# Performance work log

Measured on AMD Instinct MI355X. Metric: run time of the kernel, lower is better.

Reference implementation:

```python
import jax, jax.numpy as jnp
import numpy as np
import math

B, S, D = 16, 2048, 128
MASK_SENTINEL = -100

def setup_inputs() -> dict:
    key = jax.random.key(0)
    k1, k2, k3, k4 = jax.random.split(key, 4)
    value = jax.random.normal(k1, (B, S, D), dtype=jnp.float32)
    key_t = jax.random.normal(k2, (B, S, D), dtype=jnp.float32)
    query = jax.random.normal(k3, (B, S, D), dtype=jnp.float32)
    # mask uses -100 as the "masked out" sentinel, anything else is kept.
    bits = jax.random.randint(k4, (B, S, S), 0, 2, dtype=jnp.int32)
    mask = jnp.where(bits == 0, jnp.int32(MASK_SENTINEL), jnp.int32(0))
    return {"value": value, "key": key_t, "query": query, "mask": mask}

def reference(value, key, query, mask):
    # scores: [B, Sq, Sk]
    scale = 1.0 / math.sqrt(query.shape[-1])
    scores = jnp.einsum("bqd,bkd->bqk", query, key) * scale
    min_val = jnp.finfo(scores.dtype).min
    masked = jnp.where(mask == MASK_SENTINEL, min_val, scores)
    attn = jax.nn.softmax(masked, axis=-1)
    return jnp.einsum("bqk,bkd->bqd", attn, value)
```

## Files before the change

### kernel.cpp

```cpp
#include <hip/hip_runtime.h>
#include <hip/hip_bf16.h>

#define BATCH 16
#define SEQ   2048
#define DIM   128
#define QBLK  64
#define KVBLK 64
#define NT    (SEQ / KVBLK)
#define PPAD  72
#define L2E   1.4426950408889634f
#define THR   8.0f
#define MSENT -100

typedef __attribute__((ext_vector_type(8))) short bf16x8;
typedef __attribute__((ext_vector_type(4))) float f32x4;
typedef __attribute__((ext_vector_type(4))) int   i32x4;
typedef __attribute__((ext_vector_type(4))) unsigned u32x4;

__device__ __forceinline__ unsigned short f2bf(float f) {
  union { float f; unsigned u; } v; v.f = f;
  return (unsigned short)((v.u + 0x7FFFu + ((v.u >> 16) & 1u)) >> 16);
}
__device__ __forceinline__ unsigned packbf(float a, float b) {
  return ((unsigned)f2bf(b) << 16) | (unsigned)f2bf(a);
}

__global__ __launch_bounds__(256) void cvt_k(const float* __restrict__ K,
                                             short* __restrict__ Kb) {
  const size_t i = ((size_t)blockIdx.x * 256 + threadIdx.x) * 8;
  f32x4 a = __builtin_nontemporal_load((const f32x4*)(K + i));
  f32x4 b = __builtin_nontemporal_load((const f32x4*)(K + i + 4));
  u32x4 o = { packbf(a[0], a[1]), packbf(a[2], a[3]),
              packbf(b[0], b[1]), packbf(b[2], b[3]) };
  *(u32x4*)(Kb + i) = o;
}

__global__ __launch_bounds__(256) void cvt_vt(const float* __restrict__ V,
                                              short* __restrict__ Vt) {
  __shared__ unsigned t32[64][65];
  const int tid = threadIdx.x;
  const int b  = blockIdx.x >> 5;
  const int s0 = (blockIdx.x & 31) * 64;
  #pragma unroll
  for (int it = 0; it < 8; ++it) {
    const int idx = tid + it * 256;
    const int r = idx >> 5, c4 = idx & 31;
    f32x4 x = __builtin_nontemporal_load(
        (const f32x4*)(V + ((size_t)b * SEQ + s0 + r) * DIM + c4 * 4));
    t32[r][c4 * 2]     = packbf(x[0], x[1]);
    t32[r][c4 * 2 + 1] = packbf(x[2], x[3]);
  }
  __syncthreads();
  const int d = tid >> 1, sh = tid & 1;
  unsigned short outv[32];
  #pragma unroll
  for (int j = 0; j < 32; ++j) {
    const unsigned u = t32[sh * 32 + j][d >> 1];
    outv[j] = (d & 1) ? (unsigned short)(u >> 16) : (unsigned short)(u & 0xffff);
  }
  short* op = Vt + ((size_t)b * DIM + d) * SEQ + s0 + sh * 32;
  #pragma unroll
  for (int q = 0; q < 4; ++q) {
    bf16x8 y;
    #pragma unroll
    for (int j = 0; j < 8; ++j) y[j] = (short)outv[q * 8 + j];
    *(bf16x8*)(op + q * 8) = y;
  }
}

__device__ __forceinline__ void gload16(const void* g, void* l) {
  __builtin_amdgcn_global_load_lds(
      (const __attribute__((address_space(1))) unsigned*)g,
      (__attribute__((address_space(3))) unsigned*)l, 16, 0, 0);
}

__device__ __forceinline__ void stage_kv(const char* __restrict__ Kb2,
                                         const char* __restrict__ Vtb2,
                                         int k0, int w, int l,
                                         void* kbuf, void* vbuf) {
  #pragma unroll
  for (int it = 0; it < 4; ++it) {
    const int ch = w * 4 + it;
    const int r  = ch * 4 + (l >> 4);
    const int sg = (l & 15) ^ (r & 15);
    gload16(Kb2 + (size_t)(k0 + r) * 256 + sg * 16, (char*)kbuf + ch * 1024);
  }
  #pragma unroll
  for (int it = 0; it < 4; ++it) {
    const int ch = w * 4 + it;
    const int d2 = ch * 4 + (l >> 4);
    const int Su = (l & 15) ^ (d2 & 15);
    const int d  = 2 * d2 + (Su >> 3);
    const int m  = Su & 7;
    gload16(Vtb2 + (size_t)d * (SEQ * 2) + k0 * 2 + m * 16,
            (char*)vbuf + ch * 1024);
  }
}

__global__ __launch_bounds__(256, 2) void attn_fwd(
    const short* __restrict__ Kbf, const short* __restrict__ Vt,
    const float* __restrict__ Qg, const int* __restrict__ Mg,
    float* __restrict__ Og) {
  __shared__ short lds_k[2][KVBLK * DIM];
  __shared__ short lds_v[2][DIM * KVBLK];
  __shared__ short lds_p[4][16 * PPAD];

  const int tid = threadIdx.x;
  const int w   = tid >> 6;
  const int l   = tid & 63;
  const int g   = l >> 4;
  const int lr  = l & 15;

  const int blk = blockIdx.x;
  const int swz = (blk & 7) * 64 + (blk >> 3);
  const int b   = swz >> 5;
  const int q0  = (swz & 31) * QBLK;

  const float scale = 0.08838834764831845f;

  const char* Kb2  = (const char*)(Kbf + (size_t)b * SEQ * DIM);
  const char* Vtb2 = (const char*)(Vt  + (size_t)b * DIM * SEQ);
  const int*  Mr   = Mg + (size_t)b * SEQ * SEQ + (size_t)(q0 + w * 16 + lr) * SEQ;

  stage_kv(Kb2, Vtb2, 0, w, l, lds_k[0], lds_v[0]);
  __builtin_amdgcn_sched_barrier(0);

  bf16x8 qa[4];
  {
    const float* qbase = Qg + ((size_t)b * SEQ + (size_t)(q0 + w * 16 + lr)) * DIM + g * 8;
    #pragma unroll
    for (int kk = 0; kk < 4; ++kk) {
      f32x4 x0 = *(const f32x4*)(qbase + kk * 32);
      f32x4 x1 = *(const f32x4*)(qbase + kk * 32 + 4);
      bf16x8 f;
      #pragma unroll
      for (int j = 0; j < 4; ++j) {
        f[j]     = (short)f2bf(x0[j] * scale);
        f[j + 4] = (short)f2bf(x1[j] * scale);
      }
      qa[kk] = f;
    }
  }
  __builtin_amdgcn_sched_barrier(0);

  i32x4 mreg[4];
  #pragma unroll
  for (int sub = 0; sub < 4; ++sub)
    mreg[sub] = __builtin_nontemporal_load((const i32x4*)(Mr + 16 * sub + 4 * g));

  f32x4 acc[8];
  #pragma unroll
  for (int t = 0; t < 8; ++t) acc[t] = (f32x4){0.f, 0.f, 0.f, 0.f};
  float mrow = -1e30f, lsum = 0.f;

  asm volatile("s_waitcnt vmcnt(4)" ::: "memory");
  __builtin_amdgcn_s_barrier();

  int cur = 0;
  for (int t = 0; t < NT; ++t) {
    const int k0 = t * KVBLK;
    if (t + 1 < NT)
      stage_kv(Kb2, Vtb2, k0 + KVBLK, w, l, lds_k[cur ^ 1], lds_v[cur ^ 1]);
    __builtin_amdgcn_sched_barrier(0);

    const char* kbuf = (const char*)lds_k[cur];
    const char* vbuf = (const char*)lds_v[cur];

    f32x4 s[4];
    #pragma unroll
    for (int sub = 0; sub < 4; ++sub) s[sub] = (f32x4){0.f, 0.f, 0.f, 0.f};
    #pragma unroll
    for (int kk = 0; kk < 4; ++kk) {
      #pragma unroll
      for (int sub = 0; sub < 4; ++sub) {
        const int krow = sub * 16 + lr;
        const int cb = (64 * kk + 16 * g) ^ (lr << 4);
        bf16x8 kb = *(const bf16x8*)(kbuf + krow * 256 + cb);
        s[sub] = __builtin_amdgcn_mfma_f32_16x16x32_bf16(kb, qa[kk], s[sub], 0, 0, 0);
      }
    }

    #pragma unroll
    for (int sub = 0; sub < 4; ++sub)
      #pragma unroll
      for (int i = 0; i < 4; ++i)
        if (mreg[sub][i] == MSENT) s[sub][i] = -1e30f;
    if (t + 1 < NT) {
      #pragma unroll
      for (int sub = 0; sub < 4; ++sub)
        mreg[sub] = __builtin_nontemporal_load(
            (const i32x4*)(Mr + k0 + KVBLK + 16 * sub + 4 * g));
    }

    float tm = -1e30f;
    #pragma unroll
    for (int sub = 0; sub < 4; ++sub)
      #pragma unroll
      for (int i = 0; i < 4; ++i) tm = fmaxf(tm, s[sub][i]);
    tm = fmaxf(tm, __shfl_xor(tm, 16));
    tm = fmaxf(tm, __shfl_xor(tm, 32));
    if (__any(tm > mrow + THR)) {
      const float mnew = fmaxf(mrow, tm);
      const float al = __builtin_amdgcn_exp2f((mrow - mnew) * L2E);
      mrow = mnew; lsum *= al;
      float av[4];
      #pragma unroll
      for (int i = 0; i < 4; ++i) av[i] = __shfl(al, 4 * g + i);
      #pragma unroll
      for (int t8 = 0; t8 < 8; ++t8)
        #pragma unroll
        for (int i = 0; i < 4; ++i) acc[t8][i] *= av[i];
    }

    {
      unsigned* prow = (unsigned*)&lds_p[w][lr * PPAD];
      #pragma unroll
      for (int sub = 0; sub < 4; ++sub) {
        const float p0 = __builtin_amdgcn_exp2f((s[sub][0] - mrow) * L2E);
        const float p1 = __builtin_amdgcn_exp2f((s[sub][1] - mrow) * L2E);
        const float p2 = __builtin_amdgcn_exp2f((s[sub][2] - mrow) * L2E);
        const float p3 = __builtin_amdgcn_exp2f((s[sub][3] - mrow) * L2E);
        lsum += (p0 + p1) + (p2 + p3);
        prow[8 * sub + 2 * g]     = packbf(p0, p1);
        prow[8 * sub + 2 * g + 1] = packbf(p2, p3);
      }
    }

    bf16x8 pa[2];
    #pragma unroll
    for (int kk = 0; kk < 2; ++kk)
      pa[kk] = *(const bf16x8*)&lds_p[w][lr * PPAD + kk * 32 + g * 8];
    #pragma unroll
    for (int t8 = 0; t8 < 8; ++t8) {
      const int d2 = 8 * t8 + (lr >> 1);
      #pragma unroll
      for (int kk = 0; kk < 2; ++kk) {
        const int S = ((lr & 1) * 8 + 4 * kk + g) ^ (d2 & 15);
        bf16x8 vb = *(const bf16x8*)(vbuf + d2 * 256 + S * 16);
        acc[t8] = __builtin_amdgcn_mfma_f32_16x16x32_bf16(pa[kk], vb, acc[t8], 0, 0, 0);
      }
    }

    if (t + 1 < NT) {
      asm volatile("s_waitcnt vmcnt(4)" ::: "memory");
      __builtin_amdgcn_s_barrier();
    }
    cur ^= 1;
  }

  lsum += __shfl_xor(lsum, 16);
  lsum += __shfl_xor(lsum, 32);
  const float rden = 1.f / lsum;
  float rdv[4];
  #pragma unroll
  for (int i = 0; i < 4; ++i) rdv[i] = __shfl(rden, 4 * g + i);
  float* ob = Og + ((size_t)b * SEQ + (size_t)(q0 + w * 16)) * DIM;
  #pragma unroll
  for (int t8 = 0; t8 < 8; ++t8)
    #pragma unroll
    for (int i = 0; i < 4; ++i)
      ob[(4 * g + i) * DIM + 16 * t8 + lr] = acc[t8][i] * rdv[i];
}

extern "C" void kernel_launch(void* const* d_in, const int* in_sizes, int n_in,
                              void* d_out, int out_size, void* d_ws, size_t ws_size,
                              hipStream_t stream) {
  (void)in_sizes; (void)n_in; (void)out_size; (void)ws_size;
  const float* Vg = (const float*)d_in[0];
  const float* Kg = (const float*)d_in[1];
  const float* Qg = (const float*)d_in[2];
  const int*   Mg = (const int*)d_in[3];
  float* Og = (float*)d_out;

  short* Kbf = (short*)d_ws;
  short* Vt  = Kbf + (size_t)BATCH * SEQ * DIM;
  cvt_k<<<dim3(BATCH * SEQ * DIM / (8 * 256)), 256, 0, stream>>>(Kg, Kbf);
  cvt_vt<<<dim3(BATCH * (SEQ / 64)), 256, 0, stream>>>(Vg, Vt);
  attn_fwd<<<dim3(BATCH * (SEQ / QBLK)), 256, 0, stream>>>(Kbf, Vt, Qg, Mg, Og);
}
```

Before: 117.3 us.

## Split KV range across two blocks with merge kernel and LDS-staged mask

```diff
diff --git a/kernel.cpp b/kernel.cpp
--- a/kernel.cpp
+++ b/kernel.cpp
@@ -5,9 +5,8 @@
 #define SEQ   2048
 #define DIM   128
 #define QBLK  64
-#define KVBLK 64
-#define NT    (SEQ / KVBLK)
-#define PPAD  72
+#define KVB   32
+#define NTK   32
 #define L2E   1.4426950408889634f
 #define THR   8.0f
 #define MSENT -100
@@ -74,10 +73,218 @@
       (__attribute__((address_space(3))) unsigned*)l, 16, 0, 0);
 }
 
-__device__ __forceinline__ void stage_kv(const char* __restrict__ Kb2,
-                                         const char* __restrict__ Vtb2,
-                                         int k0, int w, int l,
-                                         void* kbuf, void* vbuf) {
+__device__ __forceinline__ void stage3(const char* __restrict__ Kb2,
+                                       const char* __restrict__ Vtb2,
+                                       const char* __restrict__ Mb2,
+                                       int k0, int w, int l,
+                                       void* kbuf, void* vbuf, void* mbuf) {
+  #pragma unroll
+  for (int it = 0; it < 2; ++it) {
+    const int ch = w * 2 + it;
+    const int r  = ch * 4 + (l >> 4);
+    const int sp = (l & 15) ^ (r & 15);
+    gload16(Kb2 + (size_t)(k0 + r) * 256 + sp * 16, (char*)kbuf + ch * 1024);
+  }
+  #pragma unroll
+  for (int it = 0; it < 2; ++it) {
+    const int ch = w * 2 + it;
+    const int d  = ch * 16 + (l >> 2);
+    const int sp = (l & 3) ^ ((l >> 3) & 3);
+    gload16(Vtb2 + (size_t)d * (SEQ * 2) + (size_t)k0 * 2 + sp * 16,
+            (char*)vbuf + ch * 1024);
+  }
+  #pragma unroll
+  for (int it = 0; it < 2; ++it) {
+    const int ch = w * 2 + it;
+    const int r  = ch * 8 + (l >> 3);
+    const int sp = (l & 7) ^ (l >> 3);
+    gload16(Mb2 + (size_t)r * (SEQ * 4) + (size_t)k0 * 4 + sp * 16,
+            (char*)mbuf + ch * 1024);
+  }
+}
+
+__global__ __launch_bounds__(256, 3) void attn_split(
+    const short* __restrict__ Kbf, const short* __restrict__ Vt,
+    const float* __restrict__ Qg, const int* __restrict__ Mg,
+    float* __restrict__ O0, float* __restrict__ O1, float2* __restrict__ ML) {
+  __shared__ short lds_k[2][KVB * DIM];
+  __shared__ short lds_v[2][DIM * KVB];
+  __shared__ int   lds_m[2][QBLK * KVB];
+
+  const int tid = threadIdx.x;
+  const int w = tid >> 6, l = tid & 63, g = l >> 4, lr = l & 15;
+
+  const int blk = blockIdx.x;
+  const int swz = (blk & 7) * 128 + (blk >> 3);
+  const int b   = swz >> 6;
+  const int x   = swz & 63;
+  const int h   = x >> 5;
+  const int q0  = (x & 31) * QBLK;
+  const int kvbase = h * (SEQ / 2);
+
+  const char* Kb2  = (const char*)(Kbf + (size_t)b * SEQ * DIM);
+  const char* Vtb2 = (const char*)(Vt  + (size_t)b * DIM * SEQ);
+  const char* Mb2  = (const char*)(Mg + (size_t)b * SEQ * SEQ + (size_t)q0 * SEQ);
+
+  stage3(Kb2, Vtb2, Mb2, kvbase, w, l, lds_k[0], lds_v[0], lds_m[0]);
+  __builtin_amdgcn_sched_barrier(0);
+
+  const float scale = 0.08838834764831845f;
+  bf16x8 qa[4];
+  {
+    const float* qbase = Qg + ((size_t)b * SEQ + (size_t)(q0 + w * 16 + lr)) * DIM + g * 8;
+    #pragma unroll
+    for (int kk = 0; kk < 4; ++kk) {
+      f32x4 x0 = *(const f32x4*)(qbase + kk * 32);
+      f32x4 x1 = *(const f32x4*)(qbase + kk * 32 + 4);
+      bf16x8 f;
+      #pragma unroll
+      for (int j = 0; j < 4; ++j) {
+        f[j]     = (short)f2bf(x0[j] * scale);
+        f[j + 4] = (short)f2bf(x1[j] * scale);
+      }
+      qa[kk] = f;
+    }
+  }
+  __builtin_amdgcn_sched_barrier(0);
+
+  f32x4 acc[8];
+  #pragma unroll
+  for (int t = 0; t < 8; ++t) acc[t] = (f32x4){0.f, 0.f, 0.f, 0.f};
+  float mrow = -1e30f, lsum = 0.f;
+
+  const int laneA = ((g & 1) << 5) + lr;
+  const int laneB = ((g & 1) << 5) + 16 + lr;
+
+  __syncthreads();
+  int cur = 0;
+
+  for (int t = 0; t < NTK; ++t) {
+    const int k0 = kvbase + t * KVB;
+    if (t + 1 < NTK)
+      stage3(Kb2, Vtb2, Mb2, k0 + KVB, w, l,
+             lds_k[cur ^ 1], lds_v[cur ^ 1], lds_m[cur ^ 1]);
+    __builtin_amdgcn_sched_barrier(0);
+
+    const char* kbuf = (const char*)lds_k[cur];
+    const char* vbuf = (const char*)lds_v[cur];
+    const char* mbuf = (const char*)lds_m[cur];
+
+    f32x4 s[2];
+    s[0] = (f32x4){0.f, 0.f, 0.f, 0.f};
+    s[1] = (f32x4){0.f, 0.f, 0.f, 0.f};
+    #pragma unroll
+    for (int kk = 0; kk < 4; ++kk) {
+      const int S = (((4 * kk + g) ^ lr) << 4);
+      bf16x8 kb0 = *(const bf16x8*)(kbuf + lr * 256 + S);
+      bf16x8 kb1 = *(const bf16x8*)(kbuf + (16 + lr) * 256 + S);
+      s[0] = __builtin_amdgcn_mfma_f32_16x16x32_bf16(kb0, qa[kk], s[0], 0, 0, 0);
+      s[1] = __builtin_amdgcn_mfma_f32_16x16x32_bf16(kb1, qa[kk], s[1], 0, 0, 0);
+    }
+
+    #pragma unroll
+    for (int sub = 0; sub < 2; ++sub) {
+      const i32x4 mm = *(const i32x4*)(
+          mbuf + (w * 16 + lr) * 128 + (((4 * sub + g) ^ (lr & 7)) << 4));
+      #pragma unroll
+      for (int i = 0; i < 4; ++i)
+        if (mm[i] == MSENT) s[sub][i] = -1e30f;
+    }
+
+    float tm = s[0][0];
+    tm = fmaxf(tm, s[0][1]); tm = fmaxf(tm, s[0][2]); tm = fmaxf(tm, s[0][3]);
+    tm = fmaxf(tm, s[1][0]); tm = fmaxf(tm, s[1][1]);
+    tm = fmaxf(tm, s[1][2]); tm = fmaxf(tm, s[1][3]);
+    tm = fmaxf(tm, __shfl_xor(tm, 16));
+    tm = fmaxf(tm, __shfl_xor(tm, 32));
+    if (__any(tm > mrow + THR)) {
+      const float mnew = fmaxf(mrow, tm);
+      const float al = __builtin_amdgcn_exp2f((mrow - mnew) * L2E);
+      mrow = mnew; lsum *= al;
+      float av[4];
+      #pragma unroll
+      for (int i = 0; i < 4; ++i) av[i] = __shfl(al, 4 * g + i);
+      #pragma unroll
+      for (int t8 = 0; t8 < 8; ++t8)
+        #pragma unroll
+        for (int i = 0; i < 4; ++i) acc[t8][i] *= av[i];
+    }
+
+    unsigned pk[2][2];
+    #pragma unroll
+    for (int sub = 0; sub < 2; ++sub) {
+      const float p0 = __builtin_amdgcn_exp2f((s[sub][0] - mrow) * L2E);
+      const float p1 = __builtin_amdgcn_exp2f((s[sub][1] - mrow) * L2E);
+      const float p2 = __builtin_amdgcn_exp2f((s[sub][2] - mrow) * L2E);
+      const float p3 = __builtin_amdgcn_exp2f((s[sub][3] - mrow) * L2E);
+      lsum += (p0 + p1) + (p2 + p3);
+      pk[sub][0] = packbf(p0, p1);
+      pk[sub][1] = packbf(p2, p3);
+    }
+    const unsigned s00 = (unsigned)__shfl((int)pk[0][0], laneA);
+    const unsigned s01 = (unsigned)__shfl((int)pk[0][1], laneA);
+    const unsigned s02 = (unsigned)__shfl((int)pk[0][0], laneB);
+    const unsigned s03 = (unsigned)__shfl((int)pk[0][1], laneB);
+    const unsigned s10 = (unsigned)__shfl((int)pk[1][0], laneA);
+    const unsigned s11 = (unsigned)__shfl((int)pk[1][1], laneA);
+    const unsigned s12 = (unsigned)__shfl((int)pk[1][0], laneB);
+    const unsigned s13 = (unsigned)__shfl((int)pk[1][1], laneB);
+    const bool hi = (g >= 2);
+    union { unsigned u[4]; bf16x8 v; } pa;
+    pa.u[0] = hi ? s10 : s00;
+    pa.u[1] = hi ? s11 : s01;
+    pa.u[2] = hi ? s12 : s02;
+    pa.u[3] = hi ? s13 : s03;
+
+    const int Sv = ((g ^ ((lr >> 1) & 3)) << 4);
+    #pragma unroll
+    for (int t8 = 0; t8 < 8; ++t8) {
+      bf16x8 vb = *(const bf16x8*)(vbuf + (16 * t8 + lr) * 64 + Sv);
+      acc[t8] = __builtin_amdgcn_mfma_f32_16x16x32_bf16(pa.v, vb, acc[t8], 0, 0, 0);
+    }
+
+    __syncthreads();
+    cur ^= 1;
+  }
+
+  lsum += __shfl_xor(lsum, 16);
+  lsum += __shfl_xor(lsum, 32);
+  if (l < 16)
+    ML[(size_t)h * (BATCH * SEQ) + (size_t)b * SEQ + q0 + w * 16 + l] =
+        make_float2(mrow, lsum);
+  float* op = (h == 0 ? O0 : O1) + ((size_t)b * SEQ + (size_t)(q0 + w * 16)) * DIM;
+  #pragma unroll
+  for (int t8 = 0; t8 < 8; ++t8)
+    #pragma unroll
+    for (int i = 0; i < 4; ++i)
+      op[(4 * g + i) * DIM + 16 * t8 + lr] = acc[t8][i];
+}
+
+__global__ __launch_bounds__(256) void merge_halves(
+    float* __restrict__ O, const float* __restrict__ O1,
+    const float2* __restrict__ ML) {
+  const int idx = blockIdx.x * 256 + threadIdx.x;
+  const int r = idx >> 5, c = (idx & 31) * 4;
+  const float2 ml0 = ML[r];
+  const float2 ml1 = ML[(size_t)BATCH * SEQ + r];
+  const float M  = fmaxf(ml0.x, ml1.x);
+  const float w0 = __builtin_amdgcn_exp2f((ml0.x - M) * L2E);
+  const float w1 = __builtin_amdgcn_exp2f((ml1.x - M) * L2E);
+  const float inv = 1.f / (w0 * ml0.y + w1 * ml1.y);
+  f32x4 o0 = *(const f32x4*)(O  + (size_t)r * DIM + c);
+  f32x4 o1 = *(const f32x4*)(O1 + (size_t)r * DIM + c);
+  f32x4 res = (o0 * w0 + o1 * w1) * inv;
+  *(f32x4*)(O + (size_t)r * DIM + c) = res;
+}
+
+#define KVBLK 64
+#define NT    (SEQ / KVBLK)
+#define PPAD  72
+
+__device__ __forceinline__ void stage_kv2(const char* __restrict__ Kb2,
+                                          const char* __restrict__ Vtb2,
+                                          int k0, int w, int l,
+                                          void* kbuf, void* vbuf) {
   #pragma unroll
   for (int it = 0; it < 4; ++it) {
     const int ch = w * 4 + it;
@@ -97,34 +304,25 @@
   }
 }
 
-__global__ __launch_bounds__(256, 2) void attn_fwd(
+__global__ __launch_bounds__(256, 2) void attn_fwd_fb(
     const short* __restrict__ Kbf, const short* __restrict__ Vt,
     const float* __restrict__ Qg, const int* __restrict__ Mg,
     float* __restrict__ Og) {
   __shared__ short lds_k[2][KVBLK * DIM];
   __shared__ short lds_v[2][DIM * KVBLK];
   __shared__ short lds_p[4][16 * PPAD];
-
   const int tid = threadIdx.x;
-  const int w   = tid >> 6;
-  const int l   = tid & 63;
-  const int g   = l >> 4;
-  const int lr  = l & 15;
-
+  const int w = tid >> 6, l = tid & 63, g = l >> 4, lr = l & 15;
   const int blk = blockIdx.x;
   const int swz = (blk & 7) * 64 + (blk >> 3);
   const int b   = swz >> 5;
   const int q0  = (swz & 31) * QBLK;
-
   const float scale = 0.08838834764831845f;
-
   const char* Kb2  = (const char*)(Kbf + (size_t)b * SEQ * DIM);
   const char* Vtb2 = (const char*)(Vt  + (size_t)b * DIM * SEQ);
   const int*  Mr   = Mg + (size_t)b * SEQ * SEQ + (size_t)(q0 + w * 16 + lr) * SEQ;
-
-  stage_kv(Kb2, Vtb2, 0, w, l, lds_k[0], lds_v[0]);
+  stage_kv2(Kb2, Vtb2, 0, w, l, lds_k[0], lds_v[0]);
   __builtin_amdgcn_sched_barrier(0);
-
   bf16x8 qa[4];
   {
     const float* qbase = Qg + ((size_t)b * SEQ + (size_t)(q0 + w * 16 + lr)) * DIM + g * 8;
@@ -135,37 +333,31 @@
       bf16x8 f;
       #pragma unroll
       for (int j = 0; j < 4; ++j) {
-        f[j]     = (short)f2bf(x0[j] * scale);
+        f[j] = (short)f2bf(x0[j] * scale);
         f[j + 4] = (short)f2bf(x1[j] * scale);
       }
       qa[kk] = f;
     }
   }
   __builtin_amdgcn_sched_barrier(0);
-
   i32x4 mreg[4];
   #pragma unroll
   for (int sub = 0; sub < 4; ++sub)
     mreg[sub] = __builtin_nontemporal_load((const i32x4*)(Mr + 16 * sub + 4 * g));
-
   f32x4 acc[8];
   #pragma unroll
   for (int t = 0; t < 8; ++t) acc[t] = (f32x4){0.f, 0.f, 0.f, 0.f};
   float mrow = -1e30f, lsum = 0.f;
-
   asm volatile("s_waitcnt vmcnt(4)" ::: "memory");
   __builtin_amdgcn_s_barrier();
-
   int cur = 0;
   for (int t = 0; t < NT; ++t) {
     const int k0 = t * KVBLK;
     if (t + 1 < NT)
-      stage_kv(Kb2, Vtb2, k0 + KVBLK, w, l, lds_k[cur ^ 1], lds_v[cur ^ 1]);
+      stage_kv2(Kb2, Vtb2, k0 + KVBLK, w, l, lds_k[cur ^ 1], lds_v[cur ^ 1]);
     __builtin_amdgcn_sched_barrier(0);
-
     const char* kbuf = (const char*)lds_k[cur];
     const char* vbuf = (const char*)lds_v[cur];
-
     f32x4 s[4];
     #pragma unroll
     for (int sub = 0; sub < 4; ++sub) s[sub] = (f32x4){0.f, 0.f, 0.f, 0.f};
@@ -179,7 +371,6 @@
         s[sub] = __builtin_amdgcn_mfma_f32_16x16x32_bf16(kb, qa[kk], s[sub], 0, 0, 0);
       }
     }
-
     #pragma unroll
     for (int sub = 0; sub < 4; ++sub)
       #pragma unroll
@@ -191,7 +382,6 @@
         mreg[sub] = __builtin_nontemporal_load(
             (const i32x4*)(Mr + k0 + KVBLK + 16 * sub + 4 * g));
     }
-
     float tm = -1e30f;
     #pragma unroll
     for (int sub = 0; sub < 4; ++sub)
@@ -211,7 +401,6 @@
         #pragma unroll
         for (int i = 0; i < 4; ++i) acc[t8][i] *= av[i];
     }
-
     {
       unsigned* prow = (unsigned*)&lds_p[w][lr * PPAD];
       #pragma unroll
@@ -225,7 +414,6 @@
         prow[8 * sub + 2 * g + 1] = packbf(p2, p3);
       }
     }
-
     bf16x8 pa[2];
     #pragma unroll
     for (int kk = 0; kk < 2; ++kk)
@@ -240,14 +428,12 @@
         acc[t8] = __builtin_amdgcn_mfma_f32_16x16x32_bf16(pa[kk], vb, acc[t8], 0, 0, 0);
       }
     }
-
     if (t + 1 < NT) {
       asm volatile("s_waitcnt vmcnt(4)" ::: "memory");
       __builtin_amdgcn_s_barrier();
     }
     cur ^= 1;
   }
-
   lsum += __shfl_xor(lsum, 16);
   lsum += __shfl_xor(lsum, 32);
   const float rden = 1.f / lsum;
@@ -265,16 +451,32 @@
 extern "C" void kernel_launch(void* const* d_in, const int* in_sizes, int n_in,
                               void* d_out, int out_size, void* d_ws, size_t ws_size,
                               hipStream_t stream) {
-  (void)in_sizes; (void)n_in; (void)out_size; (void)ws_size;
+  (void)in_sizes; (void)n_in; (void)out_size;
   const float* Vg = (const float*)d_in[0];
   const float* Kg = (const float*)d_in[1];
   const float* Qg = (const float*)d_in[2];
   const int*   Mg = (const int*)d_in[3];
   float* Og = (float*)d_out;
 
+  const size_t NE = (size_t)BATCH * SEQ * DIM;
   short* Kbf = (short*)d_ws;
-  short* Vt  = Kbf + (size_t)BATCH * SEQ * DIM;
+  short* Vt  = Kbf + NE;
+  float* O1  = (float*)(Vt + NE);
+  float2* ML = (float2*)(O1 + NE);
+  const size_t need_split = NE * 2 * sizeof(short) + NE * sizeof(float)
+                          + (size_t)2 * BATCH * SEQ * sizeof(float2);
+  const size_t need_fb    = NE * 2 * sizeof(short);
+
   cvt_k<<<dim3(BATCH * SEQ * DIM / (8 * 256)), 256, 0, stream>>>(Kg, Kbf);
   cvt_vt<<<dim3(BATCH * (SEQ / 64)), 256, 0, stream>>>(Vg, Vt);
-  attn_fwd<<<dim3(BATCH * (SEQ / QBLK)), 256, 0, stream>>>(Kbf, Vt, Qg, Mg, Og);
-}
+
+  if (ws_size >= need_split) {
+    attn_split<<<dim3(2 * BATCH * (SEQ / QBLK)), 256, 0, stream>>>(
+        Kbf, Vt, Qg, Mg, Og, O1, ML);
+    merge_halves<<<dim3(BATCH * SEQ * (DIM / 4) / 256), 256, 0, stream>>>(
+        Og, O1, ML);
+  } else if (ws_size >= need_fb) {
+    attn_fwd_fb<<<dim3(BATCH * (SEQ / QBLK)), 256, 0, stream>>>(
+        Kbf, Vt, Qg, Mg, Og);
+  }
+}
```

After: 161.0 us. 37.3% more time.

## Software-pipeline QK^T of next tile with softmax and PV of current tile

Applied to the files above, without the earlier changes.

```diff
diff --git a/kernel.cpp b/kernel.cpp
--- a/kernel.cpp
+++ b/kernel.cpp
@@ -74,10 +74,8 @@
       (__attribute__((address_space(3))) unsigned*)l, 16, 0, 0);
 }
 
-__device__ __forceinline__ void stage_kv(const char* __restrict__ Kb2,
-                                         const char* __restrict__ Vtb2,
-                                         int k0, int w, int l,
-                                         void* kbuf, void* vbuf) {
+__device__ __forceinline__ void stage_k(const char* __restrict__ Kb2,
+                                        int k0, int w, int l, void* kbuf) {
   #pragma unroll
   for (int it = 0; it < 4; ++it) {
     const int ch = w * 4 + it;
@@ -85,6 +83,9 @@
     const int sg = (l & 15) ^ (r & 15);
     gload16(Kb2 + (size_t)(k0 + r) * 256 + sg * 16, (char*)kbuf + ch * 1024);
   }
+}
+__device__ __forceinline__ void stage_v(const char* __restrict__ Vtb2,
+                                        int k0, int w, int l, void* vbuf) {
   #pragma unroll
   for (int it = 0; it < 4; ++it) {
     const int ch = w * 4 + it;
@@ -92,10 +93,92 @@
     const int Su = (l & 15) ^ (d2 & 15);
     const int d  = 2 * d2 + (Su >> 3);
     const int m  = Su & 7;
-    gload16(Vtb2 + (size_t)d * (SEQ * 2) + k0 * 2 + m * 16,
+    gload16(Vtb2 + (size_t)d * (SEQ * 2) + (size_t)k0 * 2 + m * 16,
             (char*)vbuf + ch * 1024);
   }
 }
+
+#define TILE_BODY(T, PAR, SA, SB, MA, MB)                                      \
+  {                                                                            \
+    if ((T) + 2 < NT) stage_k(Kb2, ((T) + 2) * KVBLK, w, l, lds_k[(PAR)]);     \
+    if ((T) + 1 < NT) stage_v(Vtb2, ((T) + 1) * KVBLK, w, l, lds_v[(PAR) ^ 1]);\
+    __builtin_amdgcn_sched_barrier(0);                                         \
+                  \
+    _Pragma("unroll") for (int sub = 0; sub < 4; ++sub)                        \
+        _Pragma("unroll") for (int i = 0; i < 4; ++i)                          \
+            if (MA[sub][i] == MSENT) SA[sub][i] = -1e30f;                      \
+    {                                                                          \
+      float tm = -1e30f;                                                       \
+      _Pragma("unroll") for (int sub = 0; sub < 4; ++sub)                      \
+          _Pragma("unroll") for (int i = 0; i < 4; ++i)                        \
+              tm = fmaxf(tm, SA[sub][i]);                                      \
+      tm = fmaxf(tm, __shfl_xor(tm, 16));                                      \
+      tm = fmaxf(tm, __shfl_xor(tm, 32));                                      \
+      if (__any(tm > mrow + THR)) {                                            \
+        const float mnew = fmaxf(mrow, tm);                                    \
+        const float al = __builtin_amdgcn_exp2f((mrow - mnew) * L2E);          \
+        mrow = mnew; lsum *= al;                                               \
+        float av[4];                                                           \
+        _Pragma("unroll") for (int i = 0; i < 4; ++i)                          \
+            av[i] = __shfl(al, 4 * g + i);                                     \
+        _Pragma("unroll") for (int t8 = 0; t8 < 8; ++t8)                       \
+            _Pragma("unroll") for (int i = 0; i < 4; ++i)                      \
+                acc[t8][i] *= av[i];                                           \
+      }                                                                        \
+    }                                                                          \
+           \
+    if ((T) + 1 < NT) {                                                        \
+      _Pragma("unroll") for (int sub = 0; sub < 4; ++sub)                      \
+          MB[sub] = __builtin_nontemporal_load(                                \
+              (const i32x4*)(Mr + ((T) + 1) * KVBLK + 16 * sub + 4 * g));      \
+    }                                                                          \
+               \
+    if ((T) + 1 < NT) {                                                        \
+      const char* kb_ = (const char*)lds_k[(PAR) ^ 1];                         \
+      _Pragma("unroll") for (int sub = 0; sub < 4; ++sub)                      \
+          SB[sub] = (f32x4){0.f, 0.f, 0.f, 0.f};                               \
+      __builtin_amdgcn_s_setprio(1);                                           \
+      _Pragma("unroll") for (int kk = 0; kk < 4; ++kk) {                       \
+        const int cb = (64 * kk + 16 * g) ^ (lr << 4);                         \
+        _Pragma("unroll") for (int sub = 0; sub < 4; ++sub) {                  \
+          bf16x8 kb = *(const bf16x8*)(kb_ + (sub * 16 + lr) * 256 + cb);      \
+          SB[sub] = __builtin_amdgcn_mfma_f32_16x16x32_bf16(kb, qa[kk],        \
+                                                            SB[sub], 0, 0, 0); \
+        }                                                                      \
+      }                                                                        \
+      __builtin_amdgcn_s_setprio(0);                                           \
+    }                                                                          \
+                               \
+    {                                                                          \
+      unsigned* prow = (unsigned*)&lds_p[w][lr * PPAD];                        \
+      _Pragma("unroll") for (int sub = 0; sub < 4; ++sub) {                    \
+        const float p0 = __builtin_amdgcn_exp2f((SA[sub][0] - mrow) * L2E);    \
+        const float p1 = __builtin_amdgcn_exp2f((SA[sub][1] - mrow) * L2E);    \
+        const float p2 = __builtin_amdgcn_exp2f((SA[sub][2] - mrow) * L2E);    \
+        const float p3 = __builtin_amdgcn_exp2f((SA[sub][3] - mrow) * L2E);    \
+        lsum += (p0 + p1) + (p2 + p3);                                         \
+        prow[8 * sub + 2 * g]     = packbf(p0, p1);                            \
+        prow[8 * sub + 2 * g + 1] = packbf(p2, p3);                            \
+      }                                                                        \
+      bf16x8 pa0 = *(const bf16x8*)&lds_p[w][lr * PPAD + g * 8];               \
+      bf16x8 pa1 = *(const bf16x8*)&lds_p[w][lr * PPAD + 32 + g * 8];          \
+      const char* vb_ = (const char*)lds_v[(PAR)];                             \
+      __builtin_amdgcn_s_setprio(1);                                           \
+      _Pragma("unroll") for (int t8 = 0; t8 < 8; ++t8) {                       \
+        const int d2 = 8 * t8 + (lr >> 1);                                     \
+        const int S0 = (((lr & 1) * 8 + 0 + g) ^ (d2 & 15)) * 16;              \
+        const int S1 = (((lr & 1) * 8 + 4 + g) ^ (d2 & 15)) * 16;              \
+        bf16x8 v0 = *(const bf16x8*)(vb_ + d2 * 256 + S0);                     \
+        acc[t8] = __builtin_amdgcn_mfma_f32_16x16x32_bf16(pa0, v0, acc[t8],    \
+                                                          0, 0, 0);            \
+        bf16x8 v1 = *(const bf16x8*)(vb_ + d2 * 256 + S1);                     \
+        acc[t8] = __builtin_amdgcn_mfma_f32_16x16x32_bf16(pa1, v1, acc[t8],    \
+                                                          0, 0, 0);            \
+      }                                                                        \
+      __builtin_amdgcn_s_setprio(0);                                           \
+    }                                                                          \
+    if ((T) + 1 < NT) __syncthreads();                                         \
+  }
 
 __global__ __launch_bounds__(256, 2) void attn_fwd(
     const short* __restrict__ Kbf, const short* __restrict__ Vt,
@@ -106,10 +189,7 @@
   __shared__ short lds_p[4][16 * PPAD];
 
   const int tid = threadIdx.x;
-  const int w   = tid >> 6;
-  const int l   = tid & 63;
-  const int g   = l >> 4;
-  const int lr  = l & 15;
+  const int w = tid >> 6, l = tid & 63, g = l >> 4, lr = l & 15;
 
   const int blk = blockIdx.x;
   const int swz = (blk & 7) * 64 + (blk >> 3);
@@ -122,8 +202,14 @@
   const char* Vtb2 = (const char*)(Vt  + (size_t)b * DIM * SEQ);
   const int*  Mr   = Mg + (size_t)b * SEQ * SEQ + (size_t)(q0 + w * 16 + lr) * SEQ;
 
-  stage_kv(Kb2, Vtb2, 0, w, l, lds_k[0], lds_v[0]);
+  stage_k(Kb2, 0,     w, l, lds_k[0]);
+  stage_k(Kb2, KVBLK, w, l, lds_k[1]);
+  stage_v(Vtb2, 0,    w, l, lds_v[0]);
   __builtin_amdgcn_sched_barrier(0);
+  i32x4 mA[4], mB[4];
+  #pragma unroll
+  for (int sub = 0; sub < 4; ++sub)
+    mA[sub] = __builtin_nontemporal_load((const i32x4*)(Mr + 16 * sub + 4 * g));
 
   bf16x8 qa[4];
   {
@@ -141,111 +227,34 @@
       qa[kk] = f;
     }
   }
-  __builtin_amdgcn_sched_barrier(0);
-
-  i32x4 mreg[4];
-  #pragma unroll
-  for (int sub = 0; sub < 4; ++sub)
-    mreg[sub] = __builtin_nontemporal_load((const i32x4*)(Mr + 16 * sub + 4 * g));
 
   f32x4 acc[8];
   #pragma unroll
   for (int t = 0; t < 8; ++t) acc[t] = (f32x4){0.f, 0.f, 0.f, 0.f};
   float mrow = -1e30f, lsum = 0.f;
 
-  asm volatile("s_waitcnt vmcnt(4)" ::: "memory");
-  __builtin_amdgcn_s_barrier();
-
-  int cur = 0;
-  for (int t = 0; t < NT; ++t) {
-    const int k0 = t * KVBLK;
-    if (t + 1 < NT)
-      stage_kv(Kb2, Vtb2, k0 + KVBLK, w, l, lds_k[cur ^ 1], lds_v[cur ^ 1]);
-    __builtin_amdgcn_sched_barrier(0);
-
-    const char* kbuf = (const char*)lds_k[cur];
-    const char* vbuf = (const char*)lds_v[cur];
-
-    f32x4 s[4];
-    #pragma unroll
-    for (int sub = 0; sub < 4; ++sub) s[sub] = (f32x4){0.f, 0.f, 0.f, 0.f};
+  __syncthreads();
+
+  f32x4 sA[4], sB[4];
+  #pragma unroll
+  for (int sub = 0; sub < 4; ++sub) sA[sub] = (f32x4){0.f, 0.f, 0.f, 0.f};
+  {
+    const char* kb_ = (const char*)lds_k[0];
     #pragma unroll
     for (int kk = 0; kk < 4; ++kk) {
+      const int cb = (64 * kk + 16 * g) ^ (lr << 4);
       #pragma unroll
       for (int sub = 0; sub < 4; ++sub) {
-        const int krow = sub * 16 + lr;
-        const int cb = (64 * kk + 16 * g) ^ (lr << 4);
-        bf16x8 kb = *(const bf16x8*)(kbuf + krow * 256 + cb);
-        s[sub] = __builtin_amdgcn_mfma_f32_16x16x32_bf16(kb, qa[kk], s[sub], 0, 0, 0);
+        bf16x8 kb = *(const bf16x8*)(kb_ + (sub * 16 + lr) * 256 + cb);
+        sA[sub] = __builtin_amdgcn_mfma_f32_16x16x32_bf16(kb, qa[kk], sA[sub], 0, 0, 0);
       }
     }
-
-    #pragma unroll
-    for (int sub = 0; sub < 4; ++sub)
-      #pragma unroll
-      for (int i = 0; i < 4; ++i)
-        if (mreg[sub][i] == MSENT) s[sub][i] = -1e30f;
-    if (t + 1 < NT) {
-      #pragma unroll
-      for (int sub = 0; sub < 4; ++sub)
-        mreg[sub] = __builtin_nontemporal_load(
-            (const i32x4*)(Mr + k0 + KVBLK + 16 * sub + 4 * g));
-    }
-
-    float tm = -1e30f;
-    #pragma unroll
-    for (int sub = 0; sub < 4; ++sub)
-      #pragma unroll
-      for (int i = 0; i < 4; ++i) tm = fmaxf(tm, s[sub][i]);
-    tm = fmaxf(tm, __shfl_xor(tm, 16));
-    tm = fmaxf(tm, __shfl_xor(tm, 32));
-    if (__any(tm > mrow + THR)) {
-      const float mnew = fmaxf(mrow, tm);
-      const float al = __builtin_amdgcn_exp2f((mrow - mnew) * L2E);
-      mrow = mnew; lsum *= al;
-      float av[4];
-      #pragma unroll
-      for (int i = 0; i < 4; ++i) av[i] = __shfl(al, 4 * g + i);
-      #pragma unroll
-      for (int t8 = 0; t8 < 8; ++t8)
-        #pragma unroll
-        for (int i = 0; i < 4; ++i) acc[t8][i] *= av[i];
-    }
-
-    {
-      unsigned* prow = (unsigned*)&lds_p[w][lr * PPAD];
-      #pragma unroll
-      for (int sub = 0; sub < 4; ++sub) {
-        const float p0 = __builtin_amdgcn_exp2f((s[sub][0] - mrow) * L2E);
-        const float p1 = __builtin_amdgcn_exp2f((s[sub][1] - mrow) * L2E);
-        const float p2 = __builtin_amdgcn_exp2f((s[sub][2] - mrow) * L2E);
-        const float p3 = __builtin_amdgcn_exp2f((s[sub][3] - mrow) * L2E);
-        lsum += (p0 + p1) + (p2 + p3);
-        prow[8 * sub + 2 * g]     = packbf(p0, p1);
-        prow[8 * sub + 2 * g + 1] = packbf(p2, p3);
-      }
-    }
-
-    bf16x8 pa[2];
-    #pragma unroll
-    for (int kk = 0; kk < 2; ++kk)
-      pa[kk] = *(const bf16x8*)&lds_p[w][lr * PPAD + kk * 32 + g * 8];
-    #pragma unroll
-    for (int t8 = 0; t8 < 8; ++t8) {
-      const int d2 = 8 * t8 + (lr >> 1);
-      #pragma unroll
-      for (int kk = 0; kk < 2; ++kk) {
-        const int S = ((lr & 1) * 8 + 4 * kk + g) ^ (d2 & 15);
-        bf16x8 vb = *(const bf16x8*)(vbuf + d2 * 256 + S * 16);
-        acc[t8] = __builtin_amdgcn_mfma_f32_16x16x32_bf16(pa[kk], vb, acc[t8], 0, 0, 0);
-      }
-    }
-
-    if (t + 1 < NT) {
-      asm volatile("s_waitcnt vmcnt(4)" ::: "memory");
-      __builtin_amdgcn_s_barrier();
-    }
-    cur ^= 1;
+  }
+  __syncthreads();
+
+  for (int t = 0; t < NT; t += 2) {
+    TILE_BODY(t,     0, sA, sB, mA, mB);
+    TILE_BODY(t + 1, 1, sB, sA, mB, mA);
   }
 
   lsum += __shfl_xor(lsum, 16);
```

Result: faster. 108.4 us (-7.6%).
